# Kernel tuning notes

Hardware: AMD Instinct MI355X
Metric: run time of the kernel (lower is better)

Reference implementation:

```python
import jax, jax.numpy as jnp
import numpy as np

B, S, E, H = 2, 2048, 1024, 16
D = E // H  # head_dim = 64


def setup_inputs() -> dict:
    key = jax.random.key(0)
    ks = jax.random.split(key, 6)
    sc = 0.02
    return {
        "hidden_states": jax.random.normal(ks[0], (B, S, E), dtype=jnp.float32),
        "attn_bias": jax.random.normal(ks[1], (S, S), dtype=jnp.float32) * sc,
        "Wqkv": jax.random.normal(ks[2], (E, 3 * E), dtype=jnp.float32) * sc,
        "bqkv": jax.random.normal(ks[3], (3 * E,), dtype=jnp.float32) * sc,
        "Wproj": jax.random.normal(ks[4], (E, E), dtype=jnp.float32) * sc,
        "bproj": jax.random.normal(ks[5], (E,), dtype=jnp.float32) * sc,
    }


def reference(hidden_states, attn_bias, Wqkv, bqkv, Wproj, bproj):
    b, s, e = hidden_states.shape
    qkv = hidden_states @ Wqkv + bqkv                      # [b,s,3e]
    q, k, v = jnp.split(qkv, 3, axis=-1)                   # each [b,s,e]
    cache_key, cache_value = k, v                          # kvCache
    # [b,h,s,d]
    qh = q.reshape(b, s, H, D).transpose(0, 2, 1, 3)
    kh = k.reshape(b, s, H, D).transpose(0, 2, 1, 3)
    vh = v.reshape(b, s, H, D).transpose(0, 2, 1, 3)
    scores = jnp.einsum("bhqd,bhkd->bhqk", qh, kh) / jnp.sqrt(jnp.float32(D))
    scores = scores + attn_bias[:s, :s][None, None]        # learned additive bias
    causal = jnp.tril(jnp.ones((s, s), dtype=bool))
    scores = jnp.where(causal[None, None], scores, jnp.float32(-1e9))
    attn = jax.nn.softmax(scores, axis=-1)
    ctx = jnp.einsum("bhqk,bhkd->bhqd", attn, vh)
    ctx = ctx.transpose(0, 2, 1, 3).reshape(b, s, e)
    out = ctx @ Wproj + bproj                              # resid dropout p=0 -> identity
    return (out, cache_key, cache_value)
```

## Files before the change

### kernel.cpp

```cpp
#include <hip/hip_runtime.h>

#define B_ 2
#define S_ 2048
#define E_ 1024
#define H_ 16
#define D_ 64

typedef short  s16x8 __attribute__((ext_vector_type(8)));
typedef float  f32x4 __attribute__((ext_vector_type(4)));
typedef unsigned short u16x4 __attribute__((ext_vector_type(4)));

__device__ __forceinline__ ushort f2bf(float f) {
    union { float f; unsigned u; } x; x.f = f;
    unsigned u = x.u + 0x7fffu + ((x.u >> 16) & 1u);
    return (ushort)(u >> 16);
}

__device__ __forceinline__ float fast_exp2(float x) {
    float r; asm("v_exp_f32 %0, %1" : "=v"(r) : "v"(x)); return r;
}

__global__ __launch_bounds__(256) void cvtx_kernel(
    const float* __restrict__ X, ushort* __restrict__ Xbf)
{
    int i = (blockIdx.x * 256 + threadIdx.x) * 4;
    float4 v = *(const float4*)&X[i];
    u16x4 o;
    o.x = f2bf(v.x); o.y = f2bf(v.y); o.z = f2bf(v.z); o.w = f2bf(v.w);
    *(u16x4*)&Xbf[i] = o;
}

__global__ __launch_bounds__(256) void wtrans_kernel(
    const float* __restrict__ W, ushort* __restrict__ Wt, int Kdim, int Ndim)
{
    __shared__ float tile[64][65];
    int n0 = blockIdx.x * 64, k0 = blockIdx.y * 64;
    int tid = threadIdx.x;
    int c = tid & 63;
#pragma unroll
    for (int r = tid >> 6; r < 64; r += 4)
        tile[r][c] = W[(size_t)(k0 + r) * Ndim + n0 + c];
    __syncthreads();
#pragma unroll
    for (int r = tid >> 6; r < 64; r += 4)
        Wt[(size_t)(n0 + r) * Kdim + k0 + c] = f2bf(tile[c][r]);
}

__global__ __launch_bounds__(256) void prep_bias_kernel(
    const float* __restrict__ bias, ushort* __restrict__ biasT)
{
    int L = blockIdx.x;
    int qi = (int)((sqrtf(8.0f * (float)L + 1.0f) - 1.0f) * 0.5f);
    while ((qi + 1) * (qi + 2) / 2 <= L) qi++;
    while (qi * (qi + 1) / 2 > L) qi--;
    int ki = L - qi * (qi + 1) / 2;
    int tid = threadIdx.x;
    int w = tid >> 6, quad = (tid >> 4) & 3, l15 = tid & 15;
    const float LOG2E = 1.4426950408889634f;
    s16x8 h0 = (s16x8){0,0,0,0,0,0,0,0}, h1 = (s16x8){0,0,0,0,0,0,0,0};
#pragma unroll
    for (int r = 0; r < 4; r++)
#pragma unroll
        for (int kt = 0; kt < 4; kt++) {
            float v = bias[(size_t)(qi * 64 + w * 16 + quad * 4 + r) * S_
                           + ki * 64 + kt * 16 + l15] * LOG2E;
            ushort u = f2bf(v);
            int idx = r * 4 + kt;
            if (idx < 8) h0[idx] = (short)u; else h1[idx - 8] = (short)u;
        }
    ushort* dst = &biasT[((size_t)L * 256 + tid) * 16];
    *(s16x8*)dst = h0;
    *(s16x8*)(dst + 8) = h1;
}

__global__ __launch_bounds__(256) void gemm_mfma_bt(
    const ushort* __restrict__ A,
    const ushort* __restrict__ Bt,
    const float* __restrict__ bias,
    int M, int N, int K,
    float* __restrict__ C0,
    ushort* __restrict__ Qbf, float* __restrict__ Kf32, ushort* __restrict__ Kbf,
    float* __restrict__ Vf32, int mode)
{
    __shared__ ushort As[128 * 32];
    __shared__ ushort Bs[128 * 32];
    int tid = threadIdx.x;
    int wid = tid >> 6, lane = tid & 63;
    int l15 = lane & 15, quad = lane >> 4;
    int wm = wid >> 1, wn = wid & 1;
    int row0 = blockIdx.y * 128, col0 = blockIdx.x * 128;

    int sr = wid * 16 + (lane >> 2);
    int sk = (lane & 3) * 8;

    f32x4 acc[4][4];
#pragma unroll
    for (int mt = 0; mt < 4; mt++)
#pragma unroll
        for (int nt = 0; nt < 4; nt++) acc[mt][nt] = (f32x4){0.f, 0.f, 0.f, 0.f};

    for (int k0 = 0; k0 < K; k0 += 32) {
        __syncthreads();
#pragma unroll
        for (int c = 0; c < 2; c++) {
            int r = c * 64 + sr;
            __builtin_amdgcn_global_load_lds(
                (const __attribute__((address_space(1))) unsigned int*)
                    &A[(size_t)(row0 + r) * K + k0 + sk],
                (__attribute__((address_space(3))) unsigned int*)&As[r * 32 + sk],
                16, 0, 0);
            __builtin_amdgcn_global_load_lds(
                (const __attribute__((address_space(1))) unsigned int*)
                    &Bt[(size_t)(col0 + r) * K + k0 + sk],
                (__attribute__((address_space(3))) unsigned int*)&Bs[r * 32 + sk],
                16, 0, 0);
        }
        __syncthreads();

        s16x8 af[4], bf[4];
#pragma unroll
        for (int mt = 0; mt < 4; mt++)
            af[mt] = *(const s16x8*)&As[(wm * 64 + mt * 16 + l15) * 32 + quad * 8];
#pragma unroll
        for (int nt = 0; nt < 4; nt++)
            bf[nt] = *(const s16x8*)&Bs[(wn * 64 + nt * 16 + l15) * 32 + quad * 8];
#pragma unroll
        for (int mt = 0; mt < 4; mt++)
#pragma unroll
            for (int nt = 0; nt < 4; nt++)
                acc[mt][nt] = __builtin_amdgcn_mfma_f32_16x16x32_bf16(
                    af[mt], bf[nt], acc[mt][nt], 0, 0, 0);
    }

#pragma unroll
    for (int nt = 0; nt < 4; nt++) {
        int n = col0 + wn * 64 + nt * 16 + l15;
        float bv = bias[n];
        if (mode == 1) {
            int seg = n >> 10;
            int nn = n & (E_ - 1);
#pragma unroll
            for (int mt = 0; mt < 4; mt++)
#pragma unroll
                for (int r = 0; r < 4; r++) {
                    int row = row0 + wm * 64 + mt * 16 + quad * 4 + r;
                    float v = acc[mt][nt][r] + bv;
                    size_t idx = (size_t)row * E_ + nn;
                    if (seg == 0)      Qbf[idx] = f2bf(v);
                    else if (seg == 1) { Kf32[idx] = v; Kbf[idx] = f2bf(v); }
                    else               Vf32[idx] = v;
                }
        } else {
#pragma unroll
            for (int mt = 0; mt < 4; mt++)
#pragma unroll
                for (int r = 0; r < 4; r++) {
                    int row = row0 + wm * 64 + mt * 16 + quad * 4 + r;
                    C0[(size_t)row * N + n] = acc[mt][nt][r] + bv;
                }
        }
    }
}

__global__ __launch_bounds__(256) void vtrans_kernel(
    const float* __restrict__ V, ushort* __restrict__ Vt)
{
    __shared__ float tile[64][65];
    int blk = blockIdx.x;
    int s0 = (blk & 31) * 64;
    int bh = blk >> 5;
    int b = bh >> 4, h = bh & 15;
    int tid = threadIdx.x;
    int d = tid & 63;
#pragma unroll
    for (int i = tid >> 6; i < 64; i += 4)
        tile[i][d] = V[((size_t)(b * S_ + s0 + i)) * E_ + h * 64 + d];
    __syncthreads();
    int lane = tid & 63, w = tid >> 6;
#pragma unroll
    for (int dd = w; dd < 64; dd += 4)
        Vt[((size_t)(bh * 64 + dd)) * S_ + s0 + lane] = f2bf(tile[lane][dd]);
}

__global__ __launch_bounds__(256) void attn_mfma_kernel(
    const ushort* __restrict__ Qbf,
    const ushort* __restrict__ Kbf,
    const ushort* __restrict__ Vt,
    const ushort* __restrict__ biasT,
    ushort* __restrict__ Ctx)
{
    __shared__ ushort Ks[64][64];
    __shared__ ushort Vs[64][64];
    __shared__ ushort Ps[4][16][72];

    int blk = blockIdx.x;
    int bh = blk & 31;
    int pr = blk >> 5;
    int b = bh >> 4, h = bh & 15;
    int tid = threadIdx.x;
    int wid = tid >> 6, lane = tid & 63;
    int l15 = lane & 15, quad = lane >> 4;

    int skey = tid >> 2;
    int scol = (tid & 3) * 16;
    int sc0 = ((((tid & 3) * 2) ^ (skey & 7)) * 8);
    int sc1 = sc0 ^ 8;
    const float scale_l2e = 0.18033688011112042f;

    const size_t krow = (size_t)(b * S_ + skey) * E_ + h * 64 + scol;
    const size_t vrow = (size_t)(bh * 64 + skey) * S_ + scol;

    int rc0 = (quad ^ (l15 & 7)) * 8;

    for (int half = 0; half < 2; half++) {
        int qt = half ? pr : (31 - pr);
        int q0w = qt * 64 + wid * 16;

        const size_t qbase = ((size_t)(b * S_ + q0w + l15)) * E_ + h * 64 + quad * 8;
        s16x8 qa0 = *(const s16x8*)&Qbf[qbase];
        s16x8 qa1 = *(const s16x8*)&Qbf[qbase + 32];

        f32x4 o[4];
#pragma unroll
        for (int dt = 0; dt < 4; dt++) o[dt] = (f32x4){0.f, 0.f, 0.f, 0.f};
        float lsum[4];
#pragma unroll
        for (int r = 0; r < 4; r++) lsum[r] = 0.f;

        float4 kr0 = ((const float4*)&Kbf[krow])[0];
        float4 kr1 = ((const float4*)&Kbf[krow])[1];
        float4 vr0 = ((const float4*)&Vt[vrow])[0];
        float4 vr1 = ((const float4*)&Vt[vrow])[1];
        const ushort* bt = &biasT[((size_t)(qt * (qt + 1) / 2) * 256 + tid) * 16];
        s16x8 bn0 = *(const s16x8*)bt;
        s16x8 bn1 = *(const s16x8*)(bt + 8);

        for (int t = 0; t <= qt; t++) {
            int j0 = t * 64;
            __syncthreads();
            *(float4*)&Ks[skey][sc0] = kr0;
            *(float4*)&Ks[skey][sc1] = kr1;
            *(float4*)&Vs[skey][sc0] = vr0;
            *(float4*)&Vs[skey][sc1] = vr1;
            s16x8 b0 = bn0, b1 = bn1;
            __syncthreads();

            if (t < qt) {
                int j1 = j0 + 64;
                kr0 = ((const float4*)&Kbf[krow + (size_t)j1 * E_])[0];
                kr1 = ((const float4*)&Kbf[krow + (size_t)j1 * E_])[1];
                vr0 = ((const float4*)&Vt[vrow + j1])[0];
                vr1 = ((const float4*)&Vt[vrow + j1])[1];
                const ushort* btn = bt + (size_t)(t + 1) * 4096;
                bn0 = *(const s16x8*)btn;
                bn1 = *(const s16x8*)(btn + 8);
            }

            f32x4 s[4];
#pragma unroll
            for (int kt = 0; kt < 4; kt++) {
                s16x8 kb0 = *(const s16x8*)&Ks[kt * 16 + l15][rc0];
                s16x8 kb1 = *(const s16x8*)&Ks[kt * 16 + l15][rc0 ^ 32];
                f32x4 acc = (f32x4){0.f, 0.f, 0.f, 0.f};
                acc = __builtin_amdgcn_mfma_f32_16x16x32_bf16(qa0, kb0, acc, 0, 0, 0);
                acc = __builtin_amdgcn_mfma_f32_16x16x32_bf16(qa1, kb1, acc, 0, 0, 0);
                s[kt] = acc;
            }

            bool diag = (t == qt);
#pragma unroll
            for (int r = 0; r < 4; r++) {
                int row = q0w + quad * 4 + r;
#pragma unroll
                for (int kt = 0; kt < 4; kt++) {
                    int j = j0 + kt * 16 + l15;
                    int idx = r * 4 + kt;
                    ushort ub = (ushort)((idx < 8) ? b0[idx] : b1[idx - 8]);
                    union { unsigned u; float f; } bc; bc.u = ((unsigned)ub) << 16;
                    float v = fmaf(s[kt][r], scale_l2e, bc.f);
                    float p = (diag && j > row) ? 0.f : fast_exp2(v);
                    lsum[r] += p;
                    int chunk = (kt * 2 + (l15 >> 3)) ^ quad;
                    Ps[wid][quad * 4 + r][chunk * 8 + (l15 & 7)] = f2bf(p);
                }
            }

            int cb = (quad ^ (l15 >> 2)) * 8;
            s16x8 pa0 = *(const s16x8*)&Ps[wid][l15][cb];
            s16x8 pa1 = *(const s16x8*)&Ps[wid][l15][cb + 32];
#pragma unroll
            for (int dt = 0; dt < 4; dt++) {
                s16x8 vb0 = *(const s16x8*)&Vs[dt * 16 + l15][rc0];
                s16x8 vb1 = *(const s16x8*)&Vs[dt * 16 + l15][rc0 ^ 32];
                o[dt] = __builtin_amdgcn_mfma_f32_16x16x32_bf16(pa0, vb0, o[dt], 0, 0, 0);
                o[dt] = __builtin_amdgcn_mfma_f32_16x16x32_bf16(pa1, vb1, o[dt], 0, 0, 0);
            }
        }

        float inv_l[4];
#pragma unroll
        for (int r = 0; r < 4; r++) {
            float l = lsum[r];
            l += __shfl_xor(l, 1);
            l += __shfl_xor(l, 2);
            l += __shfl_xor(l, 4);
            l += __shfl_xor(l, 8);
            inv_l[r] = 1.f / l;
        }

#pragma unroll
        for (int dt = 0; dt < 4; dt++) {
#pragma unroll
            for (int r = 0; r < 4; r++) {
                int row = q0w + quad * 4 + r;
                Ctx[((size_t)(b * S_ + row)) * E_ + h * 64 + dt * 16 + l15] =
                    f2bf(o[dt][r] * inv_l[r]);
            }
        }
    }
}

extern "C" void kernel_launch(void* const* d_in, const int* in_sizes, int n_in,
                              void* d_out, int out_size, void* d_ws, size_t ws_size,
                              hipStream_t stream) {
    const float* X     = (const float*)d_in[0];
    const float* abias = (const float*)d_in[1];
    const float* Wqkv  = (const float*)d_in[2];
    const float* bqkv  = (const float*)d_in[3];
    const float* Wproj = (const float*)d_in[4];
    const float* bproj = (const float*)d_in[5];

    const size_t plane = (size_t)B_ * S_ * E_;
    float* out  = (float*)d_out;
    float* kout = out + plane;
    float* vout = kout + plane;

    ushort* xbf    = (ushort*)d_ws;
    ushort* qbf    = xbf + plane;
    ushort* kbf    = qbf + plane;
    ushort* vt     = kbf + plane;
    ushort* ctxbf  = xbf;
    ushort* wqkvt  = vt + plane;
    ushort* wprojt = wqkvt + (size_t)3 * E_ * E_;
    ushort* biasT  = wqkvt;

    const int M = B_ * S_;

    cvtx_kernel<<<dim3(plane / 1024), 256, 0, stream>>>(X, xbf);
    wtrans_kernel<<<dim3(3 * E_ / 64, E_ / 64), 256, 0, stream>>>(Wqkv, wqkvt, E_, 3 * E_);
    wtrans_kernel<<<dim3(E_ / 64, E_ / 64), 256, 0, stream>>>(Wproj, wprojt, E_, E_);

    gemm_mfma_bt<<<dim3(3 * E_ / 128, M / 128), 256, 0, stream>>>(
        xbf, wqkvt, bqkv, M, 3 * E_, E_,
        nullptr, qbf, kout, kbf, vout, 1);

    vtrans_kernel<<<dim3(B_ * H_ * (S_ / 64)), 256, 0, stream>>>(vout, vt);

    prep_bias_kernel<<<dim3(528), 256, 0, stream>>>(abias, biasT);

    attn_mfma_kernel<<<dim3(B_ * H_ * 16), 256, 0, stream>>>(
        qbf, kbf, vt, biasT, ctxbf);

    gemm_mfma_bt<<<dim3(E_ / 128, M / 128), 256, 0, stream>>>(
        ctxbf, wprojt, bproj, M, E_, E_,
        out, nullptr, nullptr, nullptr, nullptr, 0);
}
```

Measured before the change: 235.0 us.

## Use 128-row query tiles with 32 rows per wave in attention

The attention kernel now gives each block one 128-query tile, with each wave handling 32 rows as two 16-row groups. Before, each block ran two 64-query tiles paired for causal balance. The larger tile reuses every K/V tile loaded into shared memory across twice as many query rows and reuses the K fragments across both row groups, halving K/V traffic per query. The cost is more registers per wave and some idle waves on the diagonal tiles, since the upper-half waves skip the final key block. Per-block work is balanced by ordering the blocks from large Q to small Q.

Measured after the change: 261.4 us. 11.2% more time.

```diff
diff --git a/kernel.cpp b/kernel.cpp
--- a/kernel.cpp
+++ b/kernel.cpp
@@ -191,130 +191,167 @@
 {
     __shared__ ushort Ks[64][64];
     __shared__ ushort Vs[64][64];
-    __shared__ ushort Ps[4][16][72];
+    __shared__ ushort Ps[4][32][72];
 
     int blk = blockIdx.x;
     int bh = blk & 31;
-    int pr = blk >> 5;
+    int g  = blk >> 5;
+    int Q  = (g < 8) ? (15 - g) : (g - 8);
     int b = bh >> 4, h = bh & 15;
     int tid = threadIdx.x;
     int wid = tid >> 6, lane = tid & 63;
     int l15 = lane & 15, quad = lane >> 4;
+    int hw = wid >> 1;
+    int qi64 = 2 * Q + hw;
+    int tblk = 2 * Q + 1;
 
     int skey = tid >> 2;
-    int scol = (tid & 3) * 16;
     int sc0 = ((((tid & 3) * 2) ^ (skey & 7)) * 8);
     int sc1 = sc0 ^ 8;
+    int scol = (tid & 3) * 16;
     const float scale_l2e = 0.18033688011112042f;
 
     const size_t krow = (size_t)(b * S_ + skey) * E_ + h * 64 + scol;
     const size_t vrow = (size_t)(bh * 64 + skey) * S_ + scol;
-
     int rc0 = (quad ^ (l15 & 7)) * 8;
 
-    for (int half = 0; half < 2; half++) {
-        int qt = half ? pr : (31 - pr);
-        int q0w = qt * 64 + wid * 16;
-
-        const size_t qbase = ((size_t)(b * S_ + q0w + l15)) * E_ + h * 64 + quad * 8;
-        s16x8 qa0 = *(const s16x8*)&Qbf[qbase];
-        s16x8 qa1 = *(const s16x8*)&Qbf[qbase + 32];
-
-        f32x4 o[4];
-#pragma unroll
-        for (int dt = 0; dt < 4; dt++) o[dt] = (f32x4){0.f, 0.f, 0.f, 0.f};
-        float lsum[4];
-#pragma unroll
-        for (int r = 0; r < 4; r++) lsum[r] = 0.f;
-
-        float4 kr0 = ((const float4*)&Kbf[krow])[0];
-        float4 kr1 = ((const float4*)&Kbf[krow])[1];
-        float4 vr0 = ((const float4*)&Vt[vrow])[0];
-        float4 vr1 = ((const float4*)&Vt[vrow])[1];
-        const ushort* bt = &biasT[((size_t)(qt * (qt + 1) / 2) * 256 + tid) * 16];
-        s16x8 bn0 = *(const s16x8*)bt;
-        s16x8 bn1 = *(const s16x8*)(bt + 8);
-
-        for (int t = 0; t <= qt; t++) {
-            int j0 = t * 64;
-            __syncthreads();
-            *(float4*)&Ks[skey][sc0] = kr0;
-            *(float4*)&Ks[skey][sc1] = kr1;
-            *(float4*)&Vs[skey][sc0] = vr0;
-            *(float4*)&Vs[skey][sc1] = vr1;
-            s16x8 b0 = bn0, b1 = bn1;
-            __syncthreads();
-
-            if (t < qt) {
-                int j1 = j0 + 64;
-                kr0 = ((const float4*)&Kbf[krow + (size_t)j1 * E_])[0];
-                kr1 = ((const float4*)&Kbf[krow + (size_t)j1 * E_])[1];
-                vr0 = ((const float4*)&Vt[vrow + j1])[0];
-                vr1 = ((const float4*)&Vt[vrow + j1])[1];
-                const ushort* btn = bt + (size_t)(t + 1) * 4096;
-                bn0 = *(const s16x8*)btn;
-                bn1 = *(const s16x8*)(btn + 8);
+    int q0w = Q * 128 + wid * 32;
+
+    const size_t qb0 = ((size_t)(b * S_ + q0w + l15)) * E_ + h * 64 + quad * 8;
+    s16x8 qa[2][2];
+    qa[0][0] = *(const s16x8*)&Qbf[qb0];
+    qa[0][1] = *(const s16x8*)&Qbf[qb0 + 32];
+    qa[1][0] = *(const s16x8*)&Qbf[qb0 + (size_t)16 * E_];
+    qa[1][1] = *(const s16x8*)&Qbf[qb0 + (size_t)16 * E_ + 32];
+
+    f32x4 o[2][4];
+#pragma unroll
+    for (int rg = 0; rg < 2; rg++)
+#pragma unroll
+        for (int dt = 0; dt < 4; dt++) o[rg][dt] = (f32x4){0.f, 0.f, 0.f, 0.f};
+    float lsum[2][4];
+#pragma unroll
+    for (int rg = 0; rg < 2; rg++)
+#pragma unroll
+        for (int r = 0; r < 4; r++) lsum[rg][r] = 0.f;
+
+    const ushort* bt0 = &biasT[((size_t)(qi64 * (qi64 + 1) / 2) * 256
+                                + ((wid & 1) * 2) * 64 + quad * 16 + l15) * 16];
+    const ushort* bt1 = bt0 + 1024;
+
+    float4 kr0 = ((const float4*)&Kbf[krow])[0];
+    float4 kr1 = ((const float4*)&Kbf[krow])[1];
+    float4 vr0 = ((const float4*)&Vt[vrow])[0];
+    float4 vr1 = ((const float4*)&Vt[vrow])[1];
+    s16x8 bn[2][2];
+    bn[0][0] = *(const s16x8*)bt0;       bn[0][1] = *(const s16x8*)(bt0 + 8);
+    bn[1][0] = *(const s16x8*)bt1;       bn[1][1] = *(const s16x8*)(bt1 + 8);
+
+    for (int t = 0; t <= tblk; t++) {
+        int j0 = t * 64;
+        __syncthreads();
+        *(float4*)&Ks[skey][sc0] = kr0;
+        *(float4*)&Ks[skey][sc1] = kr1;
+        *(float4*)&Vs[skey][sc0] = vr0;
+        *(float4*)&Vs[skey][sc1] = vr1;
+        s16x8 bc[2][2];
+#pragma unroll
+        for (int rg = 0; rg < 2; rg++) {
+            bc[rg][0] = bn[rg][0]; bc[rg][1] = bn[rg][1];
+        }
+        __syncthreads();
+
+        if (t < tblk) {
+            int j1 = j0 + 64;
+            kr0 = ((const float4*)&Kbf[krow + (size_t)j1 * E_])[0];
+            kr1 = ((const float4*)&Kbf[krow + (size_t)j1 * E_])[1];
+            vr0 = ((const float4*)&Vt[vrow + j1])[0];
+            vr1 = ((const float4*)&Vt[vrow + j1])[1];
+        }
+        if (t < qi64) {
+            const ushort* p0 = bt0 + (size_t)(t + 1) * 4096;
+            bn[0][0] = *(const s16x8*)p0;       bn[0][1] = *(const s16x8*)(p0 + 8);
+            const ushort* p1 = bt1 + (size_t)(t + 1) * 4096;
+            bn[1][0] = *(const s16x8*)p1;       bn[1][1] = *(const s16x8*)(p1 + 8);
+        }
+
+        if (t <= qi64) {
+            bool diag = (t == qi64);
+
+            s16x8 kb[4][2];
+#pragma unroll
+            for (int kt = 0; kt < 4; kt++) {
+                kb[kt][0] = *(const s16x8*)&Ks[kt * 16 + l15][rc0];
+                kb[kt][1] = *(const s16x8*)&Ks[kt * 16 + l15][rc0 ^ 32];
             }
 
-            f32x4 s[4];
-#pragma unroll
-            for (int kt = 0; kt < 4; kt++) {
-                s16x8 kb0 = *(const s16x8*)&Ks[kt * 16 + l15][rc0];
-                s16x8 kb1 = *(const s16x8*)&Ks[kt * 16 + l15][rc0 ^ 32];
-                f32x4 acc = (f32x4){0.f, 0.f, 0.f, 0.f};
-                acc = __builtin_amdgcn_mfma_f32_16x16x32_bf16(qa0, kb0, acc, 0, 0, 0);
-                acc = __builtin_amdgcn_mfma_f32_16x16x32_bf16(qa1, kb1, acc, 0, 0, 0);
-                s[kt] = acc;
-            }
-
-            bool diag = (t == qt);
-#pragma unroll
-            for (int r = 0; r < 4; r++) {
-                int row = q0w + quad * 4 + r;
+#pragma unroll
+            for (int rg = 0; rg < 2; rg++) {
+                f32x4 s[4];
 #pragma unroll
                 for (int kt = 0; kt < 4; kt++) {
-                    int j = j0 + kt * 16 + l15;
-                    int idx = r * 4 + kt;
-                    ushort ub = (ushort)((idx < 8) ? b0[idx] : b1[idx - 8]);
-                    union { unsigned u; float f; } bc; bc.u = ((unsigned)ub) << 16;
-                    float v = fmaf(s[kt][r], scale_l2e, bc.f);
-                    float p = (diag && j > row) ? 0.f : fast_exp2(v);
-                    lsum[r] += p;
-                    int chunk = (kt * 2 + (l15 >> 3)) ^ quad;
-                    Ps[wid][quad * 4 + r][chunk * 8 + (l15 & 7)] = f2bf(p);
+                    f32x4 acc = (f32x4){0.f, 0.f, 0.f, 0.f};
+                    acc = __builtin_amdgcn_mfma_f32_16x16x32_bf16(qa[rg][0], kb[kt][0], acc, 0, 0, 0);
+                    acc = __builtin_amdgcn_mfma_f32_16x16x32_bf16(qa[rg][1], kb[kt][1], acc, 0, 0, 0);
+                    s[kt] = acc;
+                }
+#pragma unroll
+                for (int r = 0; r < 4; r++) {
+                    int row = q0w + rg * 16 + quad * 4 + r;
+#pragma unroll
+                    for (int kt = 0; kt < 4; kt++) {
+                        int j = j0 + kt * 16 + l15;
+                        int idx = r * 4 + kt;
+                        ushort ub = (ushort)((idx < 8) ? bc[rg][0][idx] : bc[rg][1][idx - 8]);
+                        union { unsigned u; float f; } bcv; bcv.u = ((unsigned)ub) << 16;
+                        float v = fmaf(s[kt][r], scale_l2e, bcv.f);
+                        float p = (diag && j > row) ? 0.f : fast_exp2(v);
+                        lsum[rg][r] += p;
+                        int chunk = (kt * 2 + (l15 >> 3)) ^ quad;
+                        Ps[wid][rg * 16 + quad * 4 + r][chunk * 8 + (l15 & 7)] = f2bf(p);
+                    }
                 }
             }
 
             int cb = (quad ^ (l15 >> 2)) * 8;
-            s16x8 pa0 = *(const s16x8*)&Ps[wid][l15][cb];
-            s16x8 pa1 = *(const s16x8*)&Ps[wid][l15][cb + 32];
+            s16x8 pa[2][2];
+#pragma unroll
+            for (int rg = 0; rg < 2; rg++) {
+                pa[rg][0] = *(const s16x8*)&Ps[wid][rg * 16 + l15][cb];
+                pa[rg][1] = *(const s16x8*)&Ps[wid][rg * 16 + l15][cb + 32];
+            }
 #pragma unroll
             for (int dt = 0; dt < 4; dt++) {
                 s16x8 vb0 = *(const s16x8*)&Vs[dt * 16 + l15][rc0];
                 s16x8 vb1 = *(const s16x8*)&Vs[dt * 16 + l15][rc0 ^ 32];
-                o[dt] = __builtin_amdgcn_mfma_f32_16x16x32_bf16(pa0, vb0, o[dt], 0, 0, 0);
-                o[dt] = __builtin_amdgcn_mfma_f32_16x16x32_bf16(pa1, vb1, o[dt], 0, 0, 0);
+#pragma unroll
+                for (int rg = 0; rg < 2; rg++) {
+                    o[rg][dt] = __builtin_amdgcn_mfma_f32_16x16x32_bf16(pa[rg][0], vb0, o[rg][dt], 0, 0, 0);
+                    o[rg][dt] = __builtin_amdgcn_mfma_f32_16x16x32_bf16(pa[rg][1], vb1, o[rg][dt], 0, 0, 0);
+                }
             }
         }
-
+    }
+
+#pragma unroll
+    for (int rg = 0; rg < 2; rg++) {
         float inv_l[4];
 #pragma unroll
         for (int r = 0; r < 4; r++) {
-            float l = lsum[r];
+            float l = lsum[rg][r];
             l += __shfl_xor(l, 1);
             l += __shfl_xor(l, 2);
             l += __shfl_xor(l, 4);
             l += __shfl_xor(l, 8);
             inv_l[r] = 1.f / l;
         }
-
 #pragma unroll
         for (int dt = 0; dt < 4; dt++) {
 #pragma unroll
             for (int r = 0; r < 4; r++) {
-                int row = q0w + quad * 4 + r;
+                int row = q0w + rg * 16 + quad * 4 + r;
                 Ctx[((size_t)(b * S_ + row)) * E_ + h * 64 + dt * 16 + l15] =
-                    f2bf(o[dt][r] * inv_l[r]);
+                    f2bf(o[rg][dt][r] * inv_l[r]);
             }
         }
     }
@@ -358,7 +395,7 @@
 
     prep_bias_kernel<<<dim3(528), 256, 0, stream>>>(abias, biasT);
 
-    attn_mfma_kernel<<<dim3(B_ * H_ * 16), 256, 0, stream>>>(
+    attn_mfma_kernel<<<dim3(512), 256, 0, stream>>>(
         qbf, kbf, vt, biasT, ctxbf);
 
     gemm_mfma_bt<<<dim3(E_ / 128, M / 128), 256, 0, stream>>>(
```

## Fuse prep launches and pack P to bf16 with permuted V layout

Applied to the files above, without the earlier changes.

Merges the X conversion and both weight transposes into one kernel launch to cut launch overhead. In attention, each lane now packs its four probabilities into two registers with v_cvt_pk_bf16_f32 and writes them as a single 8-byte LDS store instead of sixteen scattered 2-byte stores. To make that contiguous layout match the MFMA operand order, the V transpose kernel permutes the key index within each 64-key tile, so the Ps and Vt layouts must stay in agreement. The two-element indexing consistency is the main correctness risk.

After: 226.2 us. 3.8% less time.

```diff
diff --git a/kernel.cpp b/kernel.cpp
--- a/kernel.cpp
+++ b/kernel.cpp
@@ -20,22 +20,26 @@
     float r; asm("v_exp_f32 %0, %1" : "=v"(r) : "v"(x)); return r;
 }
 
-__global__ __launch_bounds__(256) void cvtx_kernel(
-    const float* __restrict__ X, ushort* __restrict__ Xbf)
-{
-    int i = (blockIdx.x * 256 + threadIdx.x) * 4;
-    float4 v = *(const float4*)&X[i];
-    u16x4 o;
-    o.x = f2bf(v.x); o.y = f2bf(v.y); o.z = f2bf(v.z); o.w = f2bf(v.w);
-    *(u16x4*)&Xbf[i] = o;
-}
-
-__global__ __launch_bounds__(256) void wtrans_kernel(
-    const float* __restrict__ W, ushort* __restrict__ Wt, int Kdim, int Ndim)
+__global__ __launch_bounds__(256) void prep_fused_kernel(
+    const float* __restrict__ X, ushort* __restrict__ Xbf,
+    const float* __restrict__ Wqkv, ushort* __restrict__ Wqkvt,
+    const float* __restrict__ Wproj, ushort* __restrict__ Wprojt)
 {
     __shared__ float tile[64][65];
-    int n0 = blockIdx.x * 64, k0 = blockIdx.y * 64;
-    int tid = threadIdx.x;
+    int blk = blockIdx.x;
+    int tid = threadIdx.x;
+    if (blk < 4096) {
+        int i = (blk * 256 + tid) * 4;
+        float4 v = *(const float4*)&X[i];
+        u16x4 o;
+        o.x = f2bf(v.x); o.y = f2bf(v.y); o.z = f2bf(v.z); o.w = f2bf(v.w);
+        *(u16x4*)&Xbf[i] = o;
+        return;
+    }
+    const float* W; ushort* Wt; int Ndim, nb;
+    if (blk < 4096 + 768) { blk -= 4096; W = Wqkv;  Wt = Wqkvt;  Ndim = 3 * E_; nb = 48; }
+    else                  { blk -= 4864; W = Wproj; Wt = Wprojt; Ndim = E_;     nb = 16; }
+    int n0 = (blk % nb) * 64, k0 = (blk / nb) * 64;
     int c = tid & 63;
 #pragma unroll
     for (int r = tid >> 6; r < 64; r += 4)
@@ -43,7 +47,7 @@
     __syncthreads();
 #pragma unroll
     for (int r = tid >> 6; r < 64; r += 4)
-        Wt[(size_t)(n0 + r) * Kdim + k0 + c] = f2bf(tile[c][r]);
+        Wt[(size_t)(n0 + r) * E_ + k0 + c] = f2bf(tile[c][r]);
 }
 
 __global__ __launch_bounds__(256) void prep_bias_kernel(
@@ -177,9 +181,10 @@
         tile[i][d] = V[((size_t)(b * S_ + s0 + i)) * E_ + h * 64 + d];
     __syncthreads();
     int lane = tid & 63, w = tid >> 6;
+    int src = ((lane & 3) * 16) + (lane >> 2);
 #pragma unroll
     for (int dd = w; dd < 64; dd += 4)
-        Vt[((size_t)(bh * 64 + dd)) * S_ + s0 + lane] = f2bf(tile[lane][dd]);
+        Vt[((size_t)(bh * 64 + dd)) * S_ + s0 + lane] = f2bf(tile[src][dd]);
 }
 
 __global__ __launch_bounds__(256) void attn_mfma_kernel(
@@ -209,7 +214,6 @@
 
     const size_t krow = (size_t)(b * S_ + skey) * E_ + h * 64 + scol;
     const size_t vrow = (size_t)(bh * 64 + skey) * S_ + scol;
-
     int rc0 = (quad ^ (l15 & 7)) * 8;
 
     for (int half = 0; half < 2; half++) {
@@ -271,6 +275,7 @@
 #pragma unroll
             for (int r = 0; r < 4; r++) {
                 int row = q0w + quad * 4 + r;
+                float pv[4];
 #pragma unroll
                 for (int kt = 0; kt < 4; kt++) {
                     int j = j0 + kt * 16 + l15;
@@ -280,14 +285,17 @@
                     float v = fmaf(s[kt][r], scale_l2e, bc.f);
                     float p = (diag && j > row) ? 0.f : fast_exp2(v);
                     lsum[r] += p;
-                    int chunk = (kt * 2 + (l15 >> 3)) ^ quad;
-                    Ps[wid][quad * 4 + r][chunk * 8 + (l15 & 7)] = f2bf(p);
+                    pv[kt] = p;
                 }
-            }
-
-            int cb = (quad ^ (l15 >> 2)) * 8;
-            s16x8 pa0 = *(const s16x8*)&Ps[wid][l15][cb];
-            s16x8 pa1 = *(const s16x8*)&Ps[wid][l15][cb + 32];
+                unsigned w0, w1;
+                asm("v_cvt_pk_bf16_f32 %0, %1, %2" : "=v"(w0) : "v"(pv[0]), "v"(pv[1]));
+                asm("v_cvt_pk_bf16_f32 %0, %1, %2" : "=v"(w1) : "v"(pv[2]), "v"(pv[3]));
+                uint2 wv; wv.x = w0; wv.y = w1;
+                *(uint2*)&Ps[wid][quad * 4 + r][l15 * 4] = wv;
+            }
+
+            s16x8 pa0 = *(const s16x8*)&Ps[wid][l15][quad * 8];
+            s16x8 pa1 = *(const s16x8*)&Ps[wid][l15][32 + quad * 8];
 #pragma unroll
             for (int dt = 0; dt < 4; dt++) {
                 s16x8 vb0 = *(const s16x8*)&Vs[dt * 16 + l15][rc0];
@@ -346,9 +354,8 @@
 
     const int M = B_ * S_;
 
-    cvtx_kernel<<<dim3(plane / 1024), 256, 0, stream>>>(X, xbf);
-    wtrans_kernel<<<dim3(3 * E_ / 64, E_ / 64), 256, 0, stream>>>(Wqkv, wqkvt, E_, 3 * E_);
-    wtrans_kernel<<<dim3(E_ / 64, E_ / 64), 256, 0, stream>>>(Wproj, wprojt, E_, E_);
+    prep_fused_kernel<<<dim3(5120), 256, 0, stream>>>(
+        X, xbf, Wqkv, wqkvt, Wproj, wprojt);
 
     gemm_mfma_bt<<<dim3(3 * E_ / 128, M / 128), 256, 0, stream>>>(
         xbf, wqkvt, bqkv, M, 3 * E_, E_,
```
